# Kernel tuning notes

Hardware: AMD Instinct MI355X
Metric: run time of the kernel (lower is better)

Reference implementation:

```python
import jax, jax.numpy as jnp
import numpy as np

N = 100000   # nodes
E = 1600000  # edges (before self-loops)
D = 128      # feature dim (in == hidden == out)
EPS = 1e-5   # LayerNorm eps (torch default)


def setup_inputs() -> dict:
    key = jax.random.key(0)
    ks = jax.random.split(key, 6)
    x = jax.random.normal(ks[0], (N, D), dtype=jnp.float32)
    edge_row = jax.random.randint(ks[1], (E,), 0, N, dtype=jnp.int32)
    edge_col = jax.random.randint(ks[2], (E,), 0, N, dtype=jnp.int32)
    scale = 1.0 / np.sqrt(D)
    inp = {"x": x, "edge_row": edge_row, "edge_col": edge_col}
    for i, kk in zip((1, 2, 3), (ks[3], ks[4], ks[5])):
        inp[f"W{i}"] = jax.random.normal(kk, (D, D), dtype=jnp.float32) * scale
        inp[f"b{i}"] = jnp.zeros((D,), jnp.float32)
        inp[f"g{i}"] = jnp.ones((D,), jnp.float32)
        inp[f"beta{i}"] = jnp.zeros((D,), jnp.float32)
    return inp


def _layer_norm(h, g, b):
    mu = jnp.mean(h, axis=-1, keepdims=True)
    var = jnp.mean((h - mu) ** 2, axis=-1, keepdims=True)
    return (h - mu) * jax.lax.rsqrt(var + EPS) * g + b


def reference(x, W1, b1, g1, beta1, W2, b2, g2, beta2, W3, b3, g3, beta3,
              edge_row, edge_col):
    n = x.shape[0]
    # gcn_norm: add self-loops, symmetric D^-1/2 (A+I) D^-1/2
    loops = jnp.arange(n, dtype=edge_row.dtype)
    row = jnp.concatenate([edge_row, loops])  # [E+N] destination
    col = jnp.concatenate([edge_col, loops])  # [E+N] source
    deg = jax.ops.segment_sum(jnp.ones(row.shape[0], dtype=x.dtype), row,
                              num_segments=n)
    dinv = jnp.where(deg > 0, jax.lax.rsqrt(deg), 0.0)
    w = dinv[row] * dinv[col]  # [E+N] normalized edge weights

    def gcn_layer(h, W, b, g, beta):
        h = h @ W                                   # [N, D] dense GEMM
        msg = w[:, None] * h[col]                   # gather + scale
        h = jax.ops.segment_sum(msg, row, num_segments=n) + b  # spmm + bias
        return jax.nn.relu(_layer_norm(h, g, beta))  # ln -> (dropout=id) -> relu

    h = gcn_layer(x, W1, b1, g1, beta1)
    h = gcn_layer(h, W2, b2, g2, beta2)
    h = gcn_layer(h, W3, b3, g3, beta3)
    return h
```

## Files before the change

kernel.cpp:

```cpp
#include <hip/hip_runtime.h>
#include <hip/hip_bf16.h>
#include <stdint.h>

#define DD 128

typedef _Float16 f16;
typedef f16 f16x4 __attribute__((ext_vector_type(4)));
typedef f16 f16x8 __attribute__((ext_vector_type(8)));
typedef float f32x4 __attribute__((ext_vector_type(4)));

__device__ __forceinline__ unsigned packcw(int c, float w) {
  f16 h = (f16)w;
  unsigned short us;
  __builtin_memcpy(&us, &h, 2);
  return ((unsigned)us << 17) | (unsigned)c;
}
__device__ __forceinline__ float unpackw(unsigned p) {
  unsigned short us = (unsigned short)(p >> 17);
  f16 h;
  __builtin_memcpy(&h, &us, 2);
  return (float)h;
}
__device__ __forceinline__ int unpackc(unsigned p) { return (int)(p & 0x1FFFFu); }

__global__ __launch_bounds__(256) void k_zero(unsigned* degE, int n) {
  int i = blockIdx.x * 256 + threadIdx.x;
  if (i < n) degE[i] = 0u;
}

__global__ __launch_bounds__(256) void k_deg_count(const int* __restrict__ row,
                                                   unsigned* degE,
                                                   unsigned short* __restrict__ rank,
                                                   int E) {
  int e = blockIdx.x * 256 + threadIdx.x;
  if (e < E) rank[e] = (unsigned short)atomicAdd(&degE[row[e]], 1u);
}

__global__ __launch_bounds__(256) void k_scan1(const unsigned* __restrict__ degE,
                                               unsigned* __restrict__ rowptr,
                                               unsigned* __restrict__ bsum,
                                               float* __restrict__ dinv, int n) {
  __shared__ unsigned sh[256];
  int tid = threadIdx.x;
  int base = blockIdx.x * 1024 + tid * 4;
  unsigned v0 = (base + 0 < n) ? degE[base + 0] : 0u;
  unsigned v1 = (base + 1 < n) ? degE[base + 1] : 0u;
  unsigned v2 = (base + 2 < n) ? degE[base + 2] : 0u;
  unsigned v3 = (base + 3 < n) ? degE[base + 3] : 0u;
  if (base + 0 < n) dinv[base + 0] = rsqrtf((float)(v0 + 1u));
  if (base + 1 < n) dinv[base + 1] = rsqrtf((float)(v1 + 1u));
  if (base + 2 < n) dinv[base + 2] = rsqrtf((float)(v2 + 1u));
  if (base + 3 < n) dinv[base + 3] = rsqrtf((float)(v3 + 1u));
  unsigned p1 = v0, p2 = p1 + v1, p3 = p2 + v2, tot = p3 + v3;
  sh[tid] = tot;
  __syncthreads();
  for (int off = 1; off < 256; off <<= 1) {
    unsigned t = (tid >= off) ? sh[tid - off] : 0u;
    __syncthreads();
    sh[tid] += t;
    __syncthreads();
  }
  unsigned excl = sh[tid] - tot;
  if (base + 0 < n) rowptr[base + 0] = excl;
  if (base + 1 < n) rowptr[base + 1] = excl + p1;
  if (base + 2 < n) rowptr[base + 2] = excl + p2;
  if (base + 3 < n) rowptr[base + 3] = excl + p3;
  if (tid == 255) bsum[blockIdx.x] = sh[255];
}

__global__ __launch_bounds__(256) void k_scan2(const unsigned* __restrict__ bsum,
                                               unsigned* __restrict__ boff, int nb) {
  __shared__ unsigned sh[256];
  int tid = threadIdx.x;
  unsigned x = (tid < nb) ? bsum[tid] : 0u;
  sh[tid] = x;
  __syncthreads();
  for (int off = 1; off < 256; off <<= 1) {
    unsigned t = (tid >= off) ? sh[tid - off] : 0u;
    __syncthreads();
    sh[tid] += t;
    __syncthreads();
  }
  if (tid < nb) boff[tid] = sh[tid] - x;
}

__global__ __launch_bounds__(256) void k_scan3(unsigned* rowptr,
                                               const unsigned* __restrict__ boff, int n) {
  int i = blockIdx.x * 256 + threadIdx.x;
  if (i < n) rowptr[i] += boff[i >> 10];
}

__global__ __launch_bounds__(256) void k_fill(const int* __restrict__ row,
                                              const int* __restrict__ col,
                                              const unsigned short* __restrict__ rank,
                                              const float* __restrict__ dinv,
                                              const unsigned* __restrict__ rowptr,
                                              unsigned* __restrict__ ep,
                                              int E, int N) {
  const int xcd = blockIdx.x & 7;
  const int blk = blockIdx.x >> 3;
  const int r0 = (int)((size_t)N * xcd / 8);
  const int r1 = (int)((size_t)N * (xcd + 1) / 8);
  const int e0 = (int)((size_t)E * blk / 256);
  const int e1 = (int)((size_t)E * (blk + 1) / 256);
  for (int e = e0 + (int)threadIdx.x; e < e1; e += 256) {
    int r = row[e];
    if (r >= r0 && r < r1) {
      int c = col[e];
      float w = dinv[r] * dinv[c];
      ep[rowptr[r] + (unsigned)rank[e]] = packcw(c, w);
    }
  }
}

__global__ __launch_bounds__(256) void k_xcast(const float* __restrict__ X,
                                               f16* __restrict__ Y, int nv8) {
  int i = blockIdx.x * 256 + threadIdx.x;
  if (i >= nv8) return;
  f32x4 a = ((const f32x4*)X)[i * 2];
  f32x4 b = ((const f32x4*)X)[i * 2 + 1];
  f16x8 o;
#pragma unroll
  for (int j = 0; j < 4; ++j) {
    o[j] = (f16)a[j];
    o[j + 4] = (f16)b[j];
  }
  ((f16x8*)Y)[i] = o;
}

__global__ __launch_bounds__(256) void k_wt3(const float* __restrict__ W0,
                                             const float* __restrict__ W1,
                                             const float* __restrict__ W2,
                                             f16* __restrict__ T0,
                                             f16* __restrict__ T1,
                                             f16* __restrict__ T2) {
  int i = blockIdx.x * 256 + threadIdx.x;
  int m = i >> 14, j = i & 16383;
  const float* W = (m == 0) ? W0 : (m == 1) ? W1 : W2;
  f16* T = (m == 0) ? T0 : (m == 1) ? T1 : T2;
  int k = j >> 7, c = j & 127;
  T[c * 128 + k] = (f16)W[j];
}

__global__ __launch_bounds__(512, 4) void k_gemm_mfma(const f16* __restrict__ H,
                                                      const f16* __restrict__ Wt,
                                                      f16* __restrict__ O, int n) {
  __shared__ short WT[16384];
  const int tx = threadIdx.x;
  const int w = tx >> 6, l = tx & 63;
  const int cl = l & 15, lg = l >> 4;
  const int rbase = blockIdx.x * 128 + w * 16;

#pragma unroll
  for (int t4 = 0; t4 < 4; ++t4) {
    int idx = tx + t4 * 512;
    int byte = idx * 16;
    int wrow = byte >> 8;
    int off = byte & 255;
    int swz = off ^ ((wrow & 7) << 4);
    *(f16x8*)((char*)WT + wrow * 256 + swz) = *(const f16x8*)((const char*)Wt + byte);
  }

  const int arow = rbase + cl;
  const bool ok = arow < n;
  const f16* rp = H + (size_t)arow * DD + lg * 8;
  f16x8 af[4];
#pragma unroll
  for (int k0 = 0; k0 < 4; ++k0) {
    f16x8 v = {};
    if (ok) v = *(const f16x8*)(rp + k0 * 32);
    af[k0] = v;
  }
  __syncthreads();

  f32x4 acc[8] = {};
#pragma unroll
  for (int k0 = 0; k0 < 4; ++k0) {
#pragma unroll
    for (int c = 0; c < 8; ++c) {
      int col = c * 16 + cl;
      int kb = k0 * 64 + lg * 16;
      int swz = kb ^ ((col & 7) << 4);
      f16x8 bv = *(const f16x8*)((const char*)WT + col * 256 + swz);
      acc[c] = __builtin_amdgcn_mfma_f32_16x16x32_f16(af[k0], bv, acc[c], 0, 0, 0);
    }
  }

#pragma unroll
  for (int c = 0; c < 8; ++c) {
    int col = c * 16 + cl;
    f32x4 a = acc[c];
#pragma unroll
    for (int j = 0; j < 4; ++j) {
      int row = rbase + lg * 4 + j;
      if (row < n) O[(size_t)row * DD + col] = (f16)a[j];
    }
  }
}

__global__ __launch_bounds__(256) void k_agg_ln(const f16* __restrict__ T,
                                                const unsigned* __restrict__ rowptr,
                                                const unsigned* __restrict__ degE,
                                                const float* __restrict__ dinv,
                                                const unsigned* __restrict__ ep,
                                                const float* __restrict__ bias,
                                                const float* __restrict__ g,
                                                const float* __restrict__ beta,
                                                f16* __restrict__ O16,
                                                float* __restrict__ O32,
                                                int n, int wfp32) {
  const int lane = threadIdx.x & 63;
  const int wid = threadIdx.x >> 6;
  const int li = lane & 31;
  const int r = blockIdx.x * 8 + wid * 2 + (lane >> 5);
  const bool valid = r < n;
  const int rs = valid ? r : (n - 1);

  const unsigned cnt = valid ? degE[rs] : 0u;
  const float di = dinv[rs];
  unsigned e = rowptr[rs];

  unsigned cntO = (unsigned)__shfl_xor((int)cnt, 32);
  int cmw = __builtin_amdgcn_readfirstlane((int)(cnt < cntO ? cnt : cntO));

  const f16* Tl = T + li * 4;
  f16x4 sv = *(const f16x4*)(Tl + (size_t)rs * DD);
  float4 bb = *(const float4*)(bias + li * 4);
  const float ws = di * di;
  float4 a0, a1, a2, a3;
  a0.x = fmaf(ws, (float)sv[0], bb.x);
  a0.y = fmaf(ws, (float)sv[1], bb.y);
  a0.z = fmaf(ws, (float)sv[2], bb.z);
  a0.w = fmaf(ws, (float)sv[3], bb.w);
  a1 = make_float4(0.f, 0.f, 0.f, 0.f);
  a2 = a1; a3 = a1;

  int k = 0;
  unsigned m0, m1, m2, m3;
  if (cmw >= 4) { m0 = ep[e]; m1 = ep[e + 1]; m2 = ep[e + 2]; m3 = ep[e + 3]; }
  while (k + 4 <= cmw) {
    unsigned q0, q1, q2, q3;
    if (k + 8 <= cmw) {
      q0 = ep[e + 4]; q1 = ep[e + 5]; q2 = ep[e + 6]; q3 = ep[e + 7];
    }
    f16x4 u0 = *(const f16x4*)(Tl + (size_t)unpackc(m0) * DD);
    f16x4 u1 = *(const f16x4*)(Tl + (size_t)unpackc(m1) * DD);
    f16x4 u2 = *(const f16x4*)(Tl + (size_t)unpackc(m2) * DD);
    f16x4 u3 = *(const f16x4*)(Tl + (size_t)unpackc(m3) * DD);
    float w0 = unpackw(m0), w1 = unpackw(m1);
    float w2 = unpackw(m2), w3 = unpackw(m3);
    a0.x = fmaf(w0, (float)u0[0], a0.x); a0.y = fmaf(w0, (float)u0[1], a0.y);
    a0.z = fmaf(w0, (float)u0[2], a0.z); a0.w = fmaf(w0, (float)u0[3], a0.w);
    a1.x = fmaf(w1, (float)u1[0], a1.x); a1.y = fmaf(w1, (float)u1[1], a1.y);
    a1.z = fmaf(w1, (float)u1[2], a1.z); a1.w = fmaf(w1, (float)u1[3], a1.w);
    a2.x = fmaf(w2, (float)u2[0], a2.x); a2.y = fmaf(w2, (float)u2[1], a2.y);
    a2.z = fmaf(w2, (float)u2[2], a2.z); a2.w = fmaf(w2, (float)u2[3], a2.w);
    a3.x = fmaf(w3, (float)u3[0], a3.x); a3.y = fmaf(w3, (float)u3[1], a3.y);
    a3.z = fmaf(w3, (float)u3[2], a3.z); a3.w = fmaf(w3, (float)u3[3], a3.w);
    m0 = q0; m1 = q1; m2 = q2; m3 = q3;
    e += 4;
    k += 4;
  }
  for (unsigned kk = (unsigned)k; kk < cnt; ++kk, ++e) {
    unsigned m = ep[e];
    f16x4 u = *(const f16x4*)(Tl + (size_t)unpackc(m) * DD);
    float w = unpackw(m);
    a0.x = fmaf(w, (float)u[0], a0.x); a0.y = fmaf(w, (float)u[1], a0.y);
    a0.z = fmaf(w, (float)u[2], a0.z); a0.w = fmaf(w, (float)u[3], a0.w);
  }
  float4 a;
  a.x = (a0.x + a1.x) + (a2.x + a3.x);
  a.y = (a0.y + a1.y) + (a2.y + a3.y);
  a.z = (a0.z + a1.z) + (a2.z + a3.z);
  a.w = (a0.w + a1.w) + (a2.w + a3.w);

  float s = (a.x + a.y) + (a.z + a.w);
#pragma unroll
  for (int o = 16; o > 0; o >>= 1) s += __shfl_xor(s, o);
  float mu = s * (1.0f / 128.0f);
  float dx = a.x - mu, dy = a.y - mu, dz = a.z - mu, dw = a.w - mu;
  float q = (dx * dx + dy * dy) + (dz * dz + dw * dw);
#pragma unroll
  for (int o = 16; o > 0; o >>= 1) q += __shfl_xor(q, o);
  float rstd = rsqrtf(q * (1.0f / 128.0f) + 1e-5f);
  float4 gg = *(const float4*)(g + li * 4);
  float4 be4 = *(const float4*)(beta + li * 4);
  float ox = fmaxf(fmaf(dx * rstd, gg.x, be4.x), 0.f);
  float oy = fmaxf(fmaf(dy * rstd, gg.y, be4.y), 0.f);
  float oz = fmaxf(fmaf(dz * rstd, gg.z, be4.z), 0.f);
  float ow = fmaxf(fmaf(dw * rstd, gg.w, be4.w), 0.f);
  if (valid) {
    if (wfp32) {
      float4 o4 = {ox, oy, oz, ow};
      *(float4*)(O32 + (size_t)r * DD + li * 4) = o4;
    } else {
      f16x4 o4 = {(f16)ox, (f16)oy, (f16)oz, (f16)ow};
      *(f16x4*)(O16 + (size_t)r * DD + li * 4) = o4;
    }
  }
}

extern "C" void kernel_launch(void* const* d_in, const int* in_sizes, int n_in,
                              void* d_out, int out_size, void* d_ws, size_t ws_size,
                              hipStream_t stream) {
  const float* x    = (const float*)d_in[0];
  const int*   erow = (const int*)d_in[1];
  const int*   ecol = (const int*)d_in[2];
  const float* Wm[3] = {(const float*)d_in[3], (const float*)d_in[7],  (const float*)d_in[11]};
  const float* bs[3] = {(const float*)d_in[4], (const float*)d_in[8],  (const float*)d_in[12]};
  const float* gs[3] = {(const float*)d_in[5], (const float*)d_in[9],  (const float*)d_in[13]};
  const float* be[3] = {(const float*)d_in[6], (const float*)d_in[10], (const float*)d_in[14]};
  const int N = in_sizes[0] / DD;
  const int E = in_sizes[1];

  uint8_t* wp = (uint8_t*)d_ws;
  auto alloc = [&](size_t bytes) {
    uint8_t* p = wp;
    wp += (bytes + 255) & ~(size_t)255;
    return p;
  };
  unsigned*       degE   = (unsigned*)alloc((size_t)N * 4);
  float*          dinv   = (float*)alloc((size_t)N * 4);
  unsigned*       rowptr = (unsigned*)alloc((size_t)N * 4);
  unsigned*       bsum   = (unsigned*)alloc(256 * 4);
  unsigned*       boff   = (unsigned*)alloc(256 * 4);
  unsigned short* rank   = (unsigned short*)alloc((size_t)E * 2);
  unsigned*       ep     = (unsigned*)alloc((size_t)E * 4);
  f16*            A16    = (f16*)alloc((size_t)N * DD * 2);
  f16*            Hb16   = (f16*)alloc((size_t)N * DD * 2);
  f16*            X16    = (f16*)alloc((size_t)N * DD * 2);
  f16*            Wt[3];
  for (int i = 0; i < 3; ++i) Wt[i] = (f16*)alloc(DD * DD * 2);

  const int nb = (N + 1023) / 1024;

  k_zero<<<(N + 255) / 256, 256, 0, stream>>>(degE, N);
  k_deg_count<<<(E + 255) / 256, 256, 0, stream>>>(erow, degE, rank, E);
  k_scan1<<<nb, 256, 0, stream>>>(degE, rowptr, bsum, dinv, N);
  k_scan2<<<1, 256, 0, stream>>>(bsum, boff, nb);
  k_scan3<<<(N + 255) / 256, 256, 0, stream>>>(rowptr, boff, N);
  k_fill<<<2048, 256, 0, stream>>>(erow, ecol, rank, dinv, rowptr, ep, E, N);
  k_xcast<<<(N * DD / 8 + 255) / 256, 256, 0, stream>>>(x, X16, N * DD / 8);
  k_wt3<<<192, 256, 0, stream>>>(Wm[0], Wm[1], Wm[2], Wt[0], Wt[1], Wt[2]);

  const int gemm_grid = (N + 127) / 128;
  const int agg_grid  = (N + 7) / 8;

  auto layer = [&](const f16* hin, int li, int last) {
    k_gemm_mfma<<<gemm_grid, 512, 0, stream>>>(hin, Wt[li], A16, N);
    k_agg_ln<<<agg_grid, 256, 0, stream>>>(A16, rowptr, degE, dinv, ep,
                                           bs[li], gs[li], be[li],
                                           Hb16, (float*)d_out, N, last);
  };

  layer(X16, 0, 0);
  layer(Hb16, 1, 0);
  layer(Hb16, 2, 1);
}
```

Before: 499.1 us.

## Slice GEMM output into 16-column panels and split aggregation from LayerNorm

The GEMM now writes its output as eight column-sliced panels of 16 features each. Aggregation runs per slice, with 8 lanes handling one row's 16 features and each lane walking a chunk of 16 rows, so the gathered working set per slice (about 3.2 MB) can stay resident in cache. LayerNorm moves into a separate kernel that reads the sliced fp16 sums. The trade-offs are that the edge list is re-read once per slice, each gather moves only 4 bytes, there is an extra kernel launch per layer, and pre-LayerNorm values take an fp16 round trip through memory.

```diff
diff --git a/kernel.cpp b/kernel.cpp
--- a/kernel.cpp
+++ b/kernel.cpp
@@ -5,6 +5,7 @@
 #define DD 128
 
 typedef _Float16 f16;
+typedef f16 f16x2 __attribute__((ext_vector_type(2)));
 typedef f16 f16x4 __attribute__((ext_vector_type(4)));
 typedef f16 f16x8 __attribute__((ext_vector_type(8)));
 typedef float f32x4 __attribute__((ext_vector_type(4)));
@@ -188,97 +189,91 @@
 
 #pragma unroll
   for (int c = 0; c < 8; ++c) {
-    int col = c * 16 + cl;
     f32x4 a = acc[c];
 #pragma unroll
     for (int j = 0; j < 4; ++j) {
       int row = rbase + lg * 4 + j;
-      if (row < n) O[(size_t)row * DD + col] = (f16)a[j];
-    }
-  }
-}
-
-__global__ __launch_bounds__(256) void k_agg_ln(const f16* __restrict__ T,
-                                                const unsigned* __restrict__ rowptr,
-                                                const unsigned* __restrict__ degE,
-                                                const float* __restrict__ dinv,
-                                                const unsigned* __restrict__ ep,
-                                                const float* __restrict__ bias,
-                                                const float* __restrict__ g,
-                                                const float* __restrict__ beta,
-                                                f16* __restrict__ O16,
-                                                float* __restrict__ O32,
-                                                int n, int wfp32) {
+      if (row < n) O[((size_t)c * n + row) * 16 + cl] = (f16)a[j];
+    }
+  }
+}
+
+#define AGG_CHUNK 16
+__global__ __launch_bounds__(256) void k_agg(const f16* __restrict__ A,
+                                             const unsigned* __restrict__ rowptr,
+                                             const unsigned* __restrict__ degE,
+                                             const float* __restrict__ dinv,
+                                             const unsigned* __restrict__ ep,
+                                             const float* __restrict__ bias,
+                                             f16* __restrict__ S, int n) {
+  const int s = blockIdx.x & 7;
+  const int bi = blockIdx.x >> 3;
+  const int lane = threadIdx.x & 63;
+  const int wid = threadIdx.x >> 6;
+  const int gl = lane & 7;
+  const int gid = bi * 32 + wid * 8 + (lane >> 3);
+  const int rA = gid * AGG_CHUNK;
+  const f16* As = A + (size_t)s * n * 16;
+  f16* Ss = S + (size_t)s * n * 16;
+  const float2 bb = *(const float2*)(bias + s * 16 + gl * 2);
+
+  for (int nn = 0; nn < AGG_CHUNK; ++nn) {
+    int r = rA + nn;
+    if (r >= n) break;
+    unsigned e = rowptr[r];
+    const unsigned cnt = degE[r];
+    const float di = dinv[r];
+    const float ws = di * di;
+    f16x2 sv = *(const f16x2*)(As + (size_t)r * 16 + gl * 2);
+    float ax0 = fmaf(ws, (float)sv[0], bb.x);
+    float ay0 = fmaf(ws, (float)sv[1], bb.y);
+    float ax1 = 0.f, ay1 = 0.f, ax2 = 0.f, ay2 = 0.f, ax3 = 0.f, ay3 = 0.f;
+    unsigned k = 0;
+    for (; k + 4 <= cnt; k += 4, e += 4) {
+      unsigned m0 = ep[e], m1 = ep[e + 1], m2 = ep[e + 2], m3 = ep[e + 3];
+      f16x2 u0 = *(const f16x2*)(As + (size_t)unpackc(m0) * 16 + gl * 2);
+      f16x2 u1 = *(const f16x2*)(As + (size_t)unpackc(m1) * 16 + gl * 2);
+      f16x2 u2 = *(const f16x2*)(As + (size_t)unpackc(m2) * 16 + gl * 2);
+      f16x2 u3 = *(const f16x2*)(As + (size_t)unpackc(m3) * 16 + gl * 2);
+      float w0 = unpackw(m0), w1 = unpackw(m1);
+      float w2 = unpackw(m2), w3 = unpackw(m3);
+      ax0 = fmaf(w0, (float)u0[0], ax0); ay0 = fmaf(w0, (float)u0[1], ay0);
+      ax1 = fmaf(w1, (float)u1[0], ax1); ay1 = fmaf(w1, (float)u1[1], ay1);
+      ax2 = fmaf(w2, (float)u2[0], ax2); ay2 = fmaf(w2, (float)u2[1], ay2);
+      ax3 = fmaf(w3, (float)u3[0], ax3); ay3 = fmaf(w3, (float)u3[1], ay3);
+    }
+    for (; k < cnt; ++k, ++e) {
+      unsigned m = ep[e];
+      f16x2 u = *(const f16x2*)(As + (size_t)unpackc(m) * 16 + gl * 2);
+      float w = unpackw(m);
+      ax0 = fmaf(w, (float)u[0], ax0);
+      ay0 = fmaf(w, (float)u[1], ay0);
+    }
+    float ox = (ax0 + ax1) + (ax2 + ax3);
+    float oy = (ay0 + ay1) + (ay2 + ay3);
+    f16x2 o2 = {(f16)ox, (f16)oy};
+    *(f16x2*)(Ss + (size_t)r * 16 + gl * 2) = o2;
+  }
+}
+
+__global__ __launch_bounds__(256) void k_ln(const f16* __restrict__ S,
+                                            const float* __restrict__ g,
+                                            const float* __restrict__ beta,
+                                            f16* __restrict__ O16,
+                                            float* __restrict__ O32,
+                                            int n, int wfp32) {
   const int lane = threadIdx.x & 63;
   const int wid = threadIdx.x >> 6;
   const int li = lane & 31;
   const int r = blockIdx.x * 8 + wid * 2 + (lane >> 5);
-  const bool valid = r < n;
-  const int rs = valid ? r : (n - 1);
-
-  const unsigned cnt = valid ? degE[rs] : 0u;
-  const float di = dinv[rs];
-  unsigned e = rowptr[rs];
-
-  unsigned cntO = (unsigned)__shfl_xor((int)cnt, 32);
-  int cmw = __builtin_amdgcn_readfirstlane((int)(cnt < cntO ? cnt : cntO));
-
-  const f16* Tl = T + li * 4;
-  f16x4 sv = *(const f16x4*)(Tl + (size_t)rs * DD);
-  float4 bb = *(const float4*)(bias + li * 4);
-  const float ws = di * di;
-  float4 a0, a1, a2, a3;
-  a0.x = fmaf(ws, (float)sv[0], bb.x);
-  a0.y = fmaf(ws, (float)sv[1], bb.y);
-  a0.z = fmaf(ws, (float)sv[2], bb.z);
-  a0.w = fmaf(ws, (float)sv[3], bb.w);
-  a1 = make_float4(0.f, 0.f, 0.f, 0.f);
-  a2 = a1; a3 = a1;
-
-  int k = 0;
-  unsigned m0, m1, m2, m3;
-  if (cmw >= 4) { m0 = ep[e]; m1 = ep[e + 1]; m2 = ep[e + 2]; m3 = ep[e + 3]; }
-  while (k + 4 <= cmw) {
-    unsigned q0, q1, q2, q3;
-    if (k + 8 <= cmw) {
-      q0 = ep[e + 4]; q1 = ep[e + 5]; q2 = ep[e + 6]; q3 = ep[e + 7];
-    }
-    f16x4 u0 = *(const f16x4*)(Tl + (size_t)unpackc(m0) * DD);
-    f16x4 u1 = *(const f16x4*)(Tl + (size_t)unpackc(m1) * DD);
-    f16x4 u2 = *(const f16x4*)(Tl + (size_t)unpackc(m2) * DD);
-    f16x4 u3 = *(const f16x4*)(Tl + (size_t)unpackc(m3) * DD);
-    float w0 = unpackw(m0), w1 = unpackw(m1);
-    float w2 = unpackw(m2), w3 = unpackw(m3);
-    a0.x = fmaf(w0, (float)u0[0], a0.x); a0.y = fmaf(w0, (float)u0[1], a0.y);
-    a0.z = fmaf(w0, (float)u0[2], a0.z); a0.w = fmaf(w0, (float)u0[3], a0.w);
-    a1.x = fmaf(w1, (float)u1[0], a1.x); a1.y = fmaf(w1, (float)u1[1], a1.y);
-    a1.z = fmaf(w1, (float)u1[2], a1.z); a1.w = fmaf(w1, (float)u1[3], a1.w);
-    a2.x = fmaf(w2, (float)u2[0], a2.x); a2.y = fmaf(w2, (float)u2[1], a2.y);
-    a2.z = fmaf(w2, (float)u2[2], a2.z); a2.w = fmaf(w2, (float)u2[3], a2.w);
-    a3.x = fmaf(w3, (float)u3[0], a3.x); a3.y = fmaf(w3, (float)u3[1], a3.y);
-    a3.z = fmaf(w3, (float)u3[2], a3.z); a3.w = fmaf(w3, (float)u3[3], a3.w);
-    m0 = q0; m1 = q1; m2 = q2; m3 = q3;
-    e += 4;
-    k += 4;
-  }
-  for (unsigned kk = (unsigned)k; kk < cnt; ++kk, ++e) {
-    unsigned m = ep[e];
-    f16x4 u = *(const f16x4*)(Tl + (size_t)unpackc(m) * DD);
-    float w = unpackw(m);
-    a0.x = fmaf(w, (float)u[0], a0.x); a0.y = fmaf(w, (float)u[1], a0.y);
-    a0.z = fmaf(w, (float)u[2], a0.z); a0.w = fmaf(w, (float)u[3], a0.w);
-  }
-  float4 a;
-  a.x = (a0.x + a1.x) + (a2.x + a3.x);
-  a.y = (a0.y + a1.y) + (a2.y + a3.y);
-  a.z = (a0.z + a1.z) + (a2.z + a3.z);
-  a.w = (a0.w + a1.w) + (a2.w + a3.w);
-
-  float s = (a.x + a.y) + (a.z + a.w);
-#pragma unroll
-  for (int o = 16; o > 0; o >>= 1) s += __shfl_xor(s, o);
-  float mu = s * (1.0f / 128.0f);
-  float dx = a.x - mu, dy = a.y - mu, dz = a.z - mu, dw = a.w - mu;
+  if (r >= n) return;
+  f16x4 sv = *(const f16x4*)(S + ((size_t)(li >> 2) * n + r) * 16 + (li & 3) * 4);
+  float ax = (float)sv[0], ay = (float)sv[1], az = (float)sv[2], aw = (float)sv[3];
+  float ssum = (ax + ay) + (az + aw);
+#pragma unroll
+  for (int o = 16; o > 0; o >>= 1) ssum += __shfl_xor(ssum, o);
+  float mu = ssum * (1.0f / 128.0f);
+  float dx = ax - mu, dy = ay - mu, dz = az - mu, dw = aw - mu;
   float q = (dx * dx + dy * dy) + (dz * dz + dw * dw);
 #pragma unroll
   for (int o = 16; o > 0; o >>= 1) q += __shfl_xor(q, o);
@@ -289,14 +284,12 @@
   float oy = fmaxf(fmaf(dy * rstd, gg.y, be4.y), 0.f);
   float oz = fmaxf(fmaf(dz * rstd, gg.z, be4.z), 0.f);
   float ow = fmaxf(fmaf(dw * rstd, gg.w, be4.w), 0.f);
-  if (valid) {
-    if (wfp32) {
-      float4 o4 = {ox, oy, oz, ow};
-      *(float4*)(O32 + (size_t)r * DD + li * 4) = o4;
-    } else {
-      f16x4 o4 = {(f16)ox, (f16)oy, (f16)oz, (f16)ow};
-      *(f16x4*)(O16 + (size_t)r * DD + li * 4) = o4;
-    }
+  if (wfp32) {
+    float4 o4 = {ox, oy, oz, ow};
+    *(float4*)(O32 + (size_t)r * DD + li * 4) = o4;
+  } else {
+    f16x4 o4 = {(f16)ox, (f16)oy, (f16)oz, (f16)ow};
+    *(f16x4*)(O16 + (size_t)r * DD + li * 4) = o4;
   }
 }
 
@@ -326,7 +319,8 @@
   unsigned*       boff   = (unsigned*)alloc(256 * 4);
   unsigned short* rank   = (unsigned short*)alloc((size_t)E * 2);
   unsigned*       ep     = (unsigned*)alloc((size_t)E * 4);
-  f16*            A16    = (f16*)alloc((size_t)N * DD * 2);
+  f16*            A_sl   = (f16*)alloc((size_t)N * DD * 2);
+  f16*            S_sl   = (f16*)alloc((size_t)N * DD * 2);
   f16*            Hb16   = (f16*)alloc((size_t)N * DD * 2);
   f16*            X16    = (f16*)alloc((size_t)N * DD * 2);
   f16*            Wt[3];
@@ -344,13 +338,15 @@
   k_wt3<<<192, 256, 0, stream>>>(Wm[0], Wm[1], Wm[2], Wt[0], Wt[1], Wt[2]);
 
   const int gemm_grid = (N + 127) / 128;
-  const int agg_grid  = (N + 7) / 8;
+  const int groups    = (N + AGG_CHUNK - 1) / AGG_CHUNK;
+  const int bps       = (groups + 31) / 32;
+  const int agg_grid  = bps * 8;
+  const int ln_grid   = (N + 7) / 8;
 
   auto layer = [&](const f16* hin, int li, int last) {
-    k_gemm_mfma<<<gemm_grid, 512, 0, stream>>>(hin, Wt[li], A16, N);
-    k_agg_ln<<<agg_grid, 256, 0, stream>>>(A16, rowptr, degE, dinv, ep,
-                                           bs[li], gs[li], be[li],
-                                           Hb16, (float*)d_out, N, last);
+    k_gemm_mfma<<<gemm_grid, 512, 0, stream>>>(hin, Wt[li], A_sl, N);
+    k_agg<<<agg_grid, 256, 0, stream>>>(A_sl, rowptr, degE, dinv, ep, bs[li], S_sl, N);
+    k_ln<<<ln_grid, 256, 0, stream>>>(S_sl, gs[li], be[li], Hb16, (float*)d_out, N, last);
   };
 
   layer(X16, 0, 0);
```

Result: slower. 730.8 us (+46.4%).
